# Optimization experiments

Measured on AMD Instinct MI355X. Metric: run time of the kernel, lower is better.

Reference implementation:

```python
import jax, jax.numpy as jnp
import numpy as np

EPS = 1e-6  # torch.nn.PairwiseDistance default eps, added to the difference before norm
B, D, H, W = 2048, 1024, 128, 128


def setup_inputs() -> dict:
    key = jax.random.key(0)
    k1, k2 = jax.random.split(key)
    x = jax.random.normal(k1, (B, D), dtype=jnp.float32)
    # SOM codebook: [input_size, H*W], matches torch.randn(input_size, out_size[0]*out_size[1])
    weight = jax.random.normal(k2, (D, H * W), dtype=jnp.float32)
    # grid locations, row-major (x, y) as produced by get_map_index()
    gx, gy = jnp.meshgrid(jnp.arange(H), jnp.arange(W), indexing='ij')
    locations = jnp.stack([gx.ravel(), gy.ravel()], axis=1).astype(jnp.float32)  # [H*W, 2]
    return {"x": x, "weight": weight, "locations": locations}


def reference(x, weight, locations):
    # dists[b, m] = || x[b] - weight[:, m] + EPS ||_2  (PairwiseDistance p=2 semantics)
    d = x.shape[1]
    sq = (jnp.sum(x * x, axis=1, keepdims=True)          # [B, 1]
          + jnp.sum(weight * weight, axis=0)[None, :]    # [1, M]
          - 2.0 * (x @ weight)                            # [B, M] GEMM
          + 2.0 * EPS * (jnp.sum(x, axis=1, keepdims=True) - jnp.sum(weight, axis=0)[None, :])
          + d * EPS * EPS)
    dists = jnp.sqrt(jnp.maximum(sq, 0.0))                # [B, M]
    losses = jnp.min(dists, axis=1, keepdims=True)        # [B, 1]
    bmu_indexes = jnp.argmin(dists, axis=1, keepdims=True)  # [B, 1] int
    bmu_locations = locations[bmu_indexes]                 # [B, 1, 2]
    loss = jnp.sum(losses) / x.shape[0]                    # scalar mean min-distance
    return bmu_indexes, bmu_locations, loss
```

## Files before the change

kernel.cpp:

```cpp
#include <hip/hip_runtime.h>
#include <cstdint>
#include <cstddef>


#define B_  2048
#define D_  1024
#define M_  16384
#define EPS_ 1e-6f

typedef _Float16 v8h __attribute__((ext_vector_type(8)));
typedef float    v4f __attribute__((ext_vector_type(4)));

static __device__ __forceinline__ unsigned long long umin64(unsigned long long a,
                                                            unsigned long long b) {
    return a < b ? a : b;
}

static __device__ __forceinline__ size_t addr16(int r, int c) {
    return (size_t)(r >> 4) * 32768 + (size_t)(c >> 2) * 1024 +
           (size_t)(c & 3) * 256 + (size_t)(r & 15) * 16;
}

#define GLDS16(g, l)                                                            \
    __builtin_amdgcn_global_load_lds(                                           \
        (const __attribute__((address_space(1))) void*)(g),                     \
        (__attribute__((address_space(3))) void*)(l), 16, 0, 0)

__global__ __launch_bounds__(256) void prep(
    const float* __restrict__ x, const float* __restrict__ W,
    _Float16* __restrict__ xh, _Float16* __restrict__ xl,
    _Float16* __restrict__ wth, _Float16* __restrict__ wtl,
    float* __restrict__ rowTerm, float* __restrict__ colTerm,
    unsigned long long* __restrict__ keys, float* __restrict__ out)
{
    const int t = threadIdx.x;
    const int blk = blockIdx.x;
    if (blk < 256) {
        __shared__ float tile[64][65];
        __shared__ float colsq[64];
        if (t < 64) colsq[t] = 0.f;
        const int m0 = blk * 64;
        const int dloc = t >> 4, mq = (t & 15) * 4;
        const int m_local = t & 63, cp = t >> 6;
        for (int dt = 0; dt < 16; ++dt) {
            const int d0 = dt * 64;
            __syncthreads();
            #pragma unroll
            for (int s = 0; s < 4; ++s) {
                float4 v = *(const float4*)(W + (size_t)(d0 + dloc + 16 * s) * M_ + m0 + mq);
                tile[dloc + 16 * s][mq + 0] = v.x;
                tile[dloc + 16 * s][mq + 1] = v.y;
                tile[dloc + 16 * s][mq + 2] = v.z;
                tile[dloc + 16 * s][mq + 3] = v.w;
            }
            __syncthreads();
            v8h h0, l0, h1, l1;
            float part = 0.f;
            #pragma unroll
            for (int e = 0; e < 8; ++e) {
                float v = tile[16 * cp + e][m_local];
                _Float16 hi = (_Float16)v;
                h0[e] = hi; l0[e] = (_Float16)(v - (float)hi);
                part += v * v - 2.0f * EPS_ * v;
            }
            #pragma unroll
            for (int e = 0; e < 8; ++e) {
                float v = tile[16 * cp + 8 + e][m_local];
                _Float16 hi = (_Float16)v;
                h1[e] = hi; l1[e] = (_Float16)(v - (float)hi);
                part += v * v - 2.0f * EPS_ * v;
            }
            atomicAdd(&colsq[m_local], part);
            const int m  = m0 + m_local;
            const int c0 = dt * 8 + 2 * cp;
            const size_t a0 = addr16(m, c0), a1 = addr16(m, c0 + 1);
            *(v8h*)((char*)wth + a0) = h0; *(v8h*)((char*)wth + a1) = h1;
            *(v8h*)((char*)wtl + a0) = l0; *(v8h*)((char*)wtl + a1) = l1;
        }
        __syncthreads();
        if (t < 64) colTerm[m0 + t] = colsq[t];
    } else if (blk < 320) {
        __shared__ float rsum[2];
        const int rb0 = (blk - 256) * 32;
        for (int p = 0; p < 16; ++p) {
            if (t < 2) rsum[t] = 0.f;
            __syncthreads();
            const int r = rb0 + 2 * p + (t >> 7);
            const int c = t & 127;
            float4 q1 = *(const float4*)(x + (size_t)r * D_ + 8 * c);
            float4 q2 = *(const float4*)(x + (size_t)r * D_ + 8 * c + 4);
            float vv[8] = {q1.x, q1.y, q1.z, q1.w, q2.x, q2.y, q2.z, q2.w};
            v8h h, l;
            float part = 0.f;
            #pragma unroll
            for (int e = 0; e < 8; ++e) {
                _Float16 hi = (_Float16)vv[e];
                h[e] = hi; l[e] = (_Float16)(vv[e] - (float)hi);
                part += vv[e] * vv[e] + 2.0f * EPS_ * vv[e];
            }
            const size_t a = addr16(r, c);
            *(v8h*)((char*)xh + a) = h;
            *(v8h*)((char*)xl + a) = l;
            for (int off = 32; off; off >>= 1) part += __shfl_down(part, off, 64);
            if ((t & 63) == 0) atomicAdd(&rsum[t >> 7], part);
            __syncthreads();
            if ((t & 127) == 0) rowTerm[r] = rsum[t >> 7];
            __syncthreads();
        }
    } else {
        for (int i = t; i < B_; i += 256) keys[i] = ~0ull;
        if (t == 0) out[3 * B_] = 0.f;
    }
}

__global__ __launch_bounds__(256, 2) void som_mfma(
    const _Float16* __restrict__ xh, const _Float16* __restrict__ xl,
    const _Float16* __restrict__ wth, const _Float16* __restrict__ wtl,
    const float* __restrict__ rowTerm, const float* __restrict__ colTerm,
    unsigned long long* __restrict__ keys)
{
    __shared__ __align__(16) char smem[49152];
    _Float16* Ah = (_Float16*)smem;
    _Float16* Al = (_Float16*)(smem + 8192);
    _Float16* Bh = (_Float16*)(smem + 16384);
    _Float16* Bl = (_Float16*)(smem + 32768);

    const int t = threadIdx.x;
    const int g = blockIdx.x;
    const int cb = (g >> 4) * 256;
    const int rb = (g & 15) * 128;
    const int L = t & 63, w = t >> 6;
    const int wro = (w >> 1) * 64;
    const int wco = (w & 1) * 128;
    const int c16 = L & 15, kq = L >> 4;

    const int wgrp = t >> 6;
    const int lane16 = (t & 63) * 16;
    const int ldsw = wgrp * 1024;
    const size_t abase0 = (size_t)((rb >> 4) + wgrp) * 32768 + lane16;
    const size_t abase1 = abase0 + 4ull * 32768;
    const size_t bbase0 = (size_t)((cb >> 4) + wgrp) * 32768 + lane16;
    const size_t bbase1 = bbase0 + 4ull * 32768;
    const size_t bbase2 = bbase0 + 8ull * 32768;
    const size_t bbase3 = bbase0 + 12ull * 32768;

    const char* pxh = (const char*)xh;
    const char* pxl = (const char*)xl;
    const char* pwh = (const char*)wth;
    const char* pwl = (const char*)wtl;

    v4f acc[4][8];
    #pragma unroll
    for (int i = 0; i < 4; ++i)
        #pragma unroll
        for (int j = 0; j < 8; ++j) acc[i][j] = (v4f){0.f, 0.f, 0.f, 0.f};

    const int lofs = kq * 128 + c16 * 8;
    int ia[4], ibx[8];
    #pragma unroll
    for (int i = 0; i < 4; ++i) ia[i] = ((wro >> 4) + i) * 512 + lofs;
    #pragma unroll
    for (int j = 0; j < 8; ++j) ibx[j] = ((wco >> 4) + j) * 512 + lofs;

    for (int S = 0; S < 32; ++S) {
        const size_t ko = (size_t)S * 1024;
        __syncthreads();
        GLDS16(pxh + abase0 + ko, smem + ldsw);
        GLDS16(pxh + abase1 + ko, smem + 4096 + ldsw);
        GLDS16(pxl + abase0 + ko, smem + 8192 + ldsw);
        GLDS16(pxl + abase1 + ko, smem + 12288 + ldsw);
        GLDS16(pwh + bbase0 + ko, smem + 16384 + ldsw);
        GLDS16(pwh + bbase1 + ko, smem + 20480 + ldsw);
        GLDS16(pwh + bbase2 + ko, smem + 24576 + ldsw);
        GLDS16(pwh + bbase3 + ko, smem + 28672 + ldsw);
        GLDS16(pwl + bbase0 + ko, smem + 32768 + ldsw);
        GLDS16(pwl + bbase1 + ko, smem + 36864 + ldsw);
        GLDS16(pwl + bbase2 + ko, smem + 40960 + ldsw);
        GLDS16(pwl + bbase3 + ko, smem + 45056 + ldsw);
        __syncthreads();

        v8h ah[4], al4[4], bh4[4], bl4[4];
        #pragma unroll
        for (int i = 0; i < 4; ++i) {
            ah[i]  = *(const v8h*)(Ah + ia[i]);
            al4[i] = *(const v8h*)(Al + ia[i]);
        }
        #pragma unroll
        for (int j = 0; j < 4; ++j) {
            bh4[j] = *(const v8h*)(Bh + ibx[j]);
            bl4[j] = *(const v8h*)(Bl + ibx[j]);
        }
        #pragma unroll
        for (int i = 0; i < 4; ++i)
            #pragma unroll
            for (int j = 0; j < 4; ++j) {
                acc[i][j] = __builtin_amdgcn_mfma_f32_16x16x32_f16(ah[i],  bh4[j], acc[i][j], 0, 0, 0);
                acc[i][j] = __builtin_amdgcn_mfma_f32_16x16x32_f16(ah[i],  bl4[j], acc[i][j], 0, 0, 0);
                acc[i][j] = __builtin_amdgcn_mfma_f32_16x16x32_f16(al4[i], bh4[j], acc[i][j], 0, 0, 0);
            }
        #pragma unroll
        for (int j = 0; j < 4; ++j) {
            bh4[j] = *(const v8h*)(Bh + ibx[j + 4]);
            bl4[j] = *(const v8h*)(Bl + ibx[j + 4]);
        }
        #pragma unroll
        for (int i = 0; i < 4; ++i)
            #pragma unroll
            for (int j = 0; j < 4; ++j) {
                acc[i][j+4] = __builtin_amdgcn_mfma_f32_16x16x32_f16(ah[i],  bh4[j], acc[i][j+4], 0, 0, 0);
                acc[i][j+4] = __builtin_amdgcn_mfma_f32_16x16x32_f16(ah[i],  bl4[j], acc[i][j+4], 0, 0, 0);
                acc[i][j+4] = __builtin_amdgcn_mfma_f32_16x16x32_f16(al4[i], bh4[j], acc[i][j+4], 0, 0, 0);
            }
    }

    float cT[8];
    #pragma unroll
    for (int j = 0; j < 8; ++j) cT[j] = colTerm[cb + wco + j * 16 + c16];
    const float de2 = (float)D_ * EPS_ * EPS_;
    #pragma unroll
    for (int i = 0; i < 4; ++i) {
        #pragma unroll
        for (int r = 0; r < 4; ++r) {
            int row_g = rb + wro + i * 16 + kq * 4 + r;
            float rt = rowTerm[row_g];
            unsigned long long best = ~0ull;
            #pragma unroll
            for (int j = 0; j < 8; ++j) {
                float sq = rt + cT[j] - 2.0f * acc[i][j][r] + de2;
                sq = fmaxf(sq, 0.0f);
                float dist = sqrtf(sq);
                unsigned long long key =
                    ((unsigned long long)__float_as_uint(dist) << 32) |
                    (unsigned int)(cb + wco + j * 16 + c16);
                best = umin64(best, key);
            }
            #pragma unroll
            for (int m = 1; m <= 8; m <<= 1) {
                unsigned long long o =
                    (unsigned long long)__shfl_xor((long long)best, m, 64);
                best = umin64(best, o);
            }
            if (c16 == 0) atomicMin(&keys[row_g], best);
        }
    }
}

__global__ void row_stats(const float* __restrict__ x, float* __restrict__ rowTerm) {
    int b = blockIdx.x;
    const float* xr = x + (size_t)b * D_;
    int t = threadIdx.x;
    float acc = 0.f;
    for (int i = t; i < D_; i += 256) {
        float v = xr[i];
        acc += v * v + 2.0f * EPS_ * v;
    }
    for (int off = 32; off; off >>= 1) acc += __shfl_down(acc, off, 64);
    __shared__ float s[4];
    if ((t & 63) == 0) s[t >> 6] = acc;
    __syncthreads();
    if (t == 0) rowTerm[b] = s[0] + s[1] + s[2] + s[3];
}

__global__ void col_stats(const float* __restrict__ w, float* __restrict__ colTerm) {
    int m = blockIdx.x * 256 + threadIdx.x;
    int d0 = blockIdx.y * 64;
    const float* p = w + (size_t)d0 * M_ + m;
    float acc = 0.f;
    #pragma unroll 8
    for (int d = 0; d < 64; ++d) {
        float v = p[(size_t)d * M_];
        acc += v * v - 2.0f * EPS_ * v;
    }
    atomicAdd(&colTerm[m], acc);
}

__global__ __launch_bounds__(256, 2) void som_gemm(
    const float* __restrict__ A, const float* __restrict__ Wt,
    const float* __restrict__ rowTerm, const float* __restrict__ colTerm,
    unsigned long long* __restrict__ keys)
{
    __shared__ float As[8][128];
    __shared__ float Bs[8][128];
    const int t  = threadIdx.x;
    const int rb = blockIdx.y * 128;
    const int cb = blockIdx.x * 128;
    const int tx = t & 15;
    const int ty = t >> 4;
    float acc[8][8];
    #pragma unroll
    for (int i = 0; i < 8; ++i)
        #pragma unroll
        for (int j = 0; j < 8; ++j) acc[i][j] = 0.f;
    const int la_row = t >> 1, la_k = (t & 1) * 4;
    const int lb_k = t >> 5, lb_n = (t & 31) * 4;
    const float* Aptr = A + (size_t)(rb + la_row) * D_ + la_k;
    const float* Bptr = Wt + (size_t)lb_k * M_ + cb + lb_n;
    for (int k0 = 0; k0 < D_; k0 += 8) {
        float4 av = *(const float4*)(Aptr + k0);
        float4 bv = *(const float4*)(Bptr + (size_t)k0 * M_);
        __syncthreads();
        As[la_k + 0][la_row] = av.x;
        As[la_k + 1][la_row] = av.y;
        As[la_k + 2][la_row] = av.z;
        As[la_k + 3][la_row] = av.w;
        *(float4*)&Bs[lb_k][lb_n] = bv;
        __syncthreads();
        #pragma unroll
        for (int k = 0; k < 8; ++k) {
            float a[8], b[8];
            #pragma unroll
            for (int i = 0; i < 8; ++i) a[i] = As[k][ty * 8 + i];
            #pragma unroll
            for (int j = 0; j < 8; ++j) b[j] = Bs[k][tx * 8 + j];
            #pragma unroll
            for (int i = 0; i < 8; ++i)
                #pragma unroll
                for (int j = 0; j < 8; ++j) acc[i][j] += a[i] * b[j];
        }
    }
    float rT[8], cT[8];
    #pragma unroll
    for (int i = 0; i < 8; ++i) rT[i] = rowTerm[rb + ty * 8 + i];
    #pragma unroll
    for (int j = 0; j < 8; ++j) cT[j] = colTerm[cb + tx * 8 + j];
    const float de2 = (float)D_ * EPS_ * EPS_;
    #pragma unroll
    for (int i = 0; i < 8; ++i) {
        unsigned long long best = ~0ull;
        #pragma unroll
        for (int j = 0; j < 8; ++j) {
            float sq = rT[i] + cT[j] - 2.0f * acc[i][j] + de2;
            sq = fmaxf(sq, 0.0f);
            float dist = sqrtf(sq);
            unsigned long long key =
                ((unsigned long long)__float_as_uint(dist) << 32) |
                (unsigned int)(cb + tx * 8 + j);
            best = umin64(best, key);
        }
        #pragma unroll
        for (int msk = 1; msk <= 8; msk <<= 1) {
            unsigned long long o = __shfl_xor((long long)best, msk, 64);
            best = umin64(best, (unsigned long long)o);
        }
        if (tx == 0) atomicMin(&keys[rb + ty * 8 + i], best);
    }
}

__global__ void finalize(const unsigned long long* __restrict__ keys,
                         const float* __restrict__ loc,
                         float* __restrict__ out)
{
    int t = threadIdx.x;
    int r = blockIdx.x * 256 + t;
    unsigned long long k = keys[r];
    unsigned int idx = (unsigned int)(k & 0xFFFFFFFFu);
    float dist = __uint_as_float((unsigned int)(k >> 32));
    out[r] = (float)idx;
    out[B_ + 2 * r]     = loc[2 * idx];
    out[B_ + 2 * r + 1] = loc[2 * idx + 1];
    float sum = dist;
    for (int off = 32; off; off >>= 1) sum += __shfl_down(sum, off, 64);
    __shared__ float s[4];
    if ((t & 63) == 0) s[t >> 6] = sum;
    __syncthreads();
    if (t == 0) atomicAdd(&out[3 * B_], (s[0] + s[1] + s[2] + s[3]) / (float)B_);
}

extern "C" void kernel_launch(void* const* d_in, const int* in_sizes, int n_in,
                              void* d_out, int out_size, void* d_ws, size_t ws_size,
                              hipStream_t stream)
{
    const float* x   = (const float*)d_in[0];
    const float* w   = (const float*)d_in[1];
    const float* loc = (const float*)d_in[2];
    float* out = (float*)d_out;

    char* ws = (char*)d_ws;
    unsigned long long* keys = (unsigned long long*)ws;
    float* rowTerm = (float*)(ws + (16 << 10));
    float* colTerm = (float*)(ws + (24 << 10));
    _Float16* xh  = (_Float16*)(ws + (1ull << 20));
    _Float16* xl  = (_Float16*)(ws + (5ull << 20));
    _Float16* wth = (_Float16*)(ws + (9ull << 20));
    _Float16* wtl = (_Float16*)(ws + (41ull << 20));
    const size_t NEED = 73ull << 20;

    if (ws_size >= NEED) {
        prep<<<321, 256, 0, stream>>>(x, w, xh, xl, wth, wtl,
                                      rowTerm, colTerm, keys, out);
        som_mfma<<<1024, 256, 0, stream>>>(
            xh, xl, wth, wtl, rowTerm, colTerm, keys);
    } else {
        hipMemsetAsync(keys, 0xFF, B_ * sizeof(unsigned long long), stream);
        hipMemsetAsync(colTerm, 0, M_ * sizeof(float), stream);
        hipMemsetAsync(out + 3 * B_, 0, sizeof(float), stream);
        row_stats<<<B_, 256, 0, stream>>>(x, rowTerm);
        col_stats<<<dim3(M_ / 256, D_ / 64), 256, 0, stream>>>(w, colTerm);
        som_gemm<<<dim3(M_ / 128, B_ / 128), 256, 0, stream>>>(
            x, w, rowTerm, colTerm, keys);
    }
    finalize<<<8, 256, 0, stream>>>(keys, loc, out);
}
```

Baseline: 299.6 us.

## Rewrite prep transposes without LDS tiling and remap GEMM block order

The weight-conversion path drops the shared-memory transpose tile and barriers. Each thread now reads 8 strided columns of W directly and writes its hi/lo fp16 chunks, and the column sums are reduced across four wave partials in LDS instead of with atomics. The x-row path assigns half-waves to rows and reduces with xor shuffles, which removes the block-wide syncs and shared atomics. The GEMM grid mapping is also changed so that consecutive blocks cover 8 column slabs across the row tiles, aiming for better L2 reuse. The direct strided W reads may coalesce less well, although adjacent threads still read adjacent m.

After: 309.7 us. 3.4% more time.

```diff
diff --git a/kernel.cpp b/kernel.cpp
--- a/kernel.cpp
+++ b/kernel.cpp
@@ -36,76 +36,67 @@
     const int t = threadIdx.x;
     const int blk = blockIdx.x;
     if (blk < 256) {
-        __shared__ float tile[64][65];
-        __shared__ float colsq[64];
-        if (t < 64) colsq[t] = 0.f;
-        const int m0 = blk * 64;
-        const int dloc = t >> 4, mq = (t & 15) * 4;
-        const int m_local = t & 63, cp = t >> 6;
-        for (int dt = 0; dt < 16; ++dt) {
-            const int d0 = dt * 64;
-            __syncthreads();
-            #pragma unroll
-            for (int s = 0; s < 4; ++s) {
-                float4 v = *(const float4*)(W + (size_t)(d0 + dloc + 16 * s) * M_ + m0 + mq);
-                tile[dloc + 16 * s][mq + 0] = v.x;
-                tile[dloc + 16 * s][mq + 1] = v.y;
-                tile[dloc + 16 * s][mq + 2] = v.z;
-                tile[dloc + 16 * s][mq + 3] = v.w;
-            }
-            __syncthreads();
-            v8h h0, l0, h1, l1;
-            float part = 0.f;
-            #pragma unroll
-            for (int e = 0; e < 8; ++e) {
-                float v = tile[16 * cp + e][m_local];
-                _Float16 hi = (_Float16)v;
-                h0[e] = hi; l0[e] = (_Float16)(v - (float)hi);
-                part += v * v - 2.0f * EPS_ * v;
-            }
-            #pragma unroll
-            for (int e = 0; e < 8; ++e) {
-                float v = tile[16 * cp + 8 + e][m_local];
-                _Float16 hi = (_Float16)v;
-                h1[e] = hi; l1[e] = (_Float16)(v - (float)hi);
-                part += v * v - 2.0f * EPS_ * v;
-            }
-            atomicAdd(&colsq[m_local], part);
-            const int m  = m0 + m_local;
-            const int c0 = dt * 8 + 2 * cp;
-            const size_t a0 = addr16(m, c0), a1 = addr16(m, c0 + 1);
-            *(v8h*)((char*)wth + a0) = h0; *(v8h*)((char*)wth + a1) = h1;
-            *(v8h*)((char*)wtl + a0) = l0; *(v8h*)((char*)wtl + a1) = l1;
-        }
-        __syncthreads();
-        if (t < 64) colTerm[m0 + t] = colsq[t];
-    } else if (blk < 320) {
-        __shared__ float rsum[2];
-        const int rb0 = (blk - 256) * 32;
-        for (int p = 0; p < 16; ++p) {
-            if (t < 2) rsum[t] = 0.f;
-            __syncthreads();
-            const int r = rb0 + 2 * p + (t >> 7);
-            const int c = t & 127;
-            float4 q1 = *(const float4*)(x + (size_t)r * D_ + 8 * c);
-            float4 q2 = *(const float4*)(x + (size_t)r * D_ + 8 * c + 4);
-            float vv[8] = {q1.x, q1.y, q1.z, q1.w, q2.x, q2.y, q2.z, q2.w};
+        __shared__ float cpart[4][64];
+        const int m_local = t & 63;
+        const int wq = t >> 6;
+        const int m = blk * 64 + m_local;
+        const float* wp = W + m;
+        const int cbase = wq * 32;
+        float part = 0.f;
+        #pragma unroll 4
+        for (int cl = 0; cl < 32; ++cl) {
+            const int c = cbase + cl;
+            const int d0 = c * 8;
+            float vv[8];
+            #pragma unroll
+            for (int e = 0; e < 8; ++e)
+                vv[e] = wp[(size_t)(d0 + e) * M_];
             v8h h, l;
-            float part = 0.f;
             #pragma unroll
             for (int e = 0; e < 8; ++e) {
                 _Float16 hi = (_Float16)vv[e];
                 h[e] = hi; l[e] = (_Float16)(vv[e] - (float)hi);
-                part += vv[e] * vv[e] + 2.0f * EPS_ * vv[e];
-            }
-            const size_t a = addr16(r, c);
-            *(v8h*)((char*)xh + a) = h;
-            *(v8h*)((char*)xl + a) = l;
-            for (int off = 32; off; off >>= 1) part += __shfl_down(part, off, 64);
-            if ((t & 63) == 0) atomicAdd(&rsum[t >> 7], part);
-            __syncthreads();
-            if ((t & 127) == 0) rowTerm[r] = rsum[t >> 7];
-            __syncthreads();
+                part += vv[e] * vv[e] - 2.0f * EPS_ * vv[e];
+            }
+            const size_t a = addr16(m, c);
+            *(v8h*)((char*)wth + a) = h;
+            *(v8h*)((char*)wtl + a) = l;
+        }
+        cpart[wq][m_local] = part;
+        __syncthreads();
+        if (t < 64)
+            colTerm[blk * 64 + t] =
+                cpart[0][t] + cpart[1][t] + cpart[2][t] + cpart[3][t];
+    } else if (blk < 320) {
+        const int rb0 = (blk - 256) * 32;
+        const int w = t >> 6, L = t & 63;
+        const int hl = L & 31;
+        #pragma unroll
+        for (int p = 0; p < 4; ++p) {
+            const int r = rb0 + 8 * p + 2 * w + (L >> 5);
+            const float* xr = x + (size_t)r * D_;
+            float part = 0.f;
+            #pragma unroll
+            for (int i = 0; i < 4; ++i) {
+                const int c = 32 * i + hl;
+                float4 q1 = *(const float4*)(xr + 8 * c);
+                float4 q2 = *(const float4*)(xr + 8 * c + 4);
+                float vv[8] = {q1.x, q1.y, q1.z, q1.w, q2.x, q2.y, q2.z, q2.w};
+                v8h h, l;
+                #pragma unroll
+                for (int e = 0; e < 8; ++e) {
+                    _Float16 hi = (_Float16)vv[e];
+                    h[e] = hi; l[e] = (_Float16)(vv[e] - (float)hi);
+                    part += vv[e] * vv[e] + 2.0f * EPS_ * vv[e];
+                }
+                const size_t a = addr16(r, c);
+                *(v8h*)((char*)xh + a) = h;
+                *(v8h*)((char*)xl + a) = l;
+            }
+            #pragma unroll
+            for (int msk = 1; msk <= 16; msk <<= 1)
+                part += __shfl_xor(part, msk, 64);
+            if (hl == 0) rowTerm[r] = part;
         }
     } else {
         for (int i = t; i < B_; i += 256) keys[i] = ~0ull;
@@ -127,8 +118,9 @@
 
     const int t = threadIdx.x;
     const int g = blockIdx.x;
-    const int cb = (g >> 4) * 256;
-    const int rb = (g & 15) * 128;
+    const int slab = (g & 7) + 8 * (g >> 7);
+    const int cb = slab * 256;
+    const int rb = ((g >> 3) & 15) * 128;
     const int L = t & 63, w = t >> 6;
     const int wro = (w >> 1) * 64;
     const int wco = (w & 1) * 128;
```
